# Optimization experiments

Measured on AMD Instinct MI355X. Metric: run time of the kernel, lower is better.

## Reference

```python
import jax, jax.numpy as jnp
import numpy as np

NEG_SLOPE = 0.2
N, E, R = 50000, 400000, 500
IN, HID, H, OUT = 128, 64, 4, 128


def _gatv2_layer(x, src, dst, e_emb, Wl, bl, Wr, br, att, bias, heads, ch, concat):
    """PyG GATv2Conv (eval mode, add_self_loops=True, fill_value=0.0)."""
    n = x.shape[0]
    xl = (x @ Wl + bl).reshape(n, heads, ch)   # source transform
    xr = (x @ Wr + br).reshape(n, heads, ch)   # destination transform
    loop = jnp.arange(n)
    src_f = jnp.concatenate([src, loop])       # self-loops appended
    dst_f = jnp.concatenate([dst, loop])
    # self-loop edge_attr is fill_value=0.0 -> lin_edge (no bias) gives 0 embedding
    e_f = jnp.concatenate([e_emb, jnp.zeros((n, heads, ch), x.dtype)], axis=0)
    m = jax.nn.leaky_relu(xl[src_f] + xr[dst_f] + e_f, NEG_SLOPE)  # [Ef,H,C]
    logits = jnp.einsum('ehc,hc->eh', m, att)
    # segment softmax over destination nodes (every node has a self loop)
    mx = jax.ops.segment_max(logits, dst_f, num_segments=n)
    a = jnp.exp(logits - mx[dst_f])
    denom = jax.ops.segment_sum(a, dst_f, num_segments=n)
    alpha = a / denom[dst_f]                                        # [Ef,H]
    out = jax.ops.segment_sum(alpha[..., None] * xl[src_f], dst_f, num_segments=n)
    if concat:
        out = out.reshape(n, heads * ch)
    else:
        out = out.mean(axis=1)
    return out + bias


def setup_inputs() -> dict:
    key = jax.random.key(0)
    ks = jax.random.split(key, 20)
    s = 0.05
    inp = {
        'x': jax.random.normal(ks[0], (N, IN), jnp.float32),
        'edge_index': jnp.stack([
            jax.random.randint(ks[1], (E,), 0, N),
            jax.random.randint(ks[2], (E,), 0, R),
            jax.random.randint(ks[3], (E,), 0, N),
        ]).astype(jnp.int64) if jax.config.jax_enable_x64 else jnp.stack([
            jax.random.randint(ks[1], (E,), 0, N),
            jax.random.randint(ks[2], (E,), 0, R),
            jax.random.randint(ks[3], (E,), 0, N),
        ]),
        'relations': jax.random.normal(ks[4], (R, IN), jnp.float32),
        # layer 1: IN -> H*HID, concat=True
        'Wl1': jax.random.normal(ks[5], (IN, H * HID), jnp.float32) * s,
        'bl1': jnp.zeros((H * HID,), jnp.float32),
        'Wr1': jax.random.normal(ks[6], (IN, H * HID), jnp.float32) * s,
        'br1': jnp.zeros((H * HID,), jnp.float32),
        'We1': jax.random.normal(ks[7], (IN, H * HID), jnp.float32) * s,
        'att1': jax.random.normal(ks[8], (H, HID), jnp.float32) * s,
        'bias1': jnp.zeros((H * HID,), jnp.float32),
        # layer 2: H*HID -> OUT, concat=False (mean over heads)
        'Wl2': jax.random.normal(ks[9], (H * HID, H * OUT), jnp.float32) * s,
        'bl2': jnp.zeros((H * OUT,), jnp.float32),
        'Wr2': jax.random.normal(ks[10], (H * HID, H * OUT), jnp.float32) * s,
        'br2': jnp.zeros((H * OUT,), jnp.float32),
        'We2': jax.random.normal(ks[11], (IN, H * OUT), jnp.float32) * s,
        'att2': jax.random.normal(ks[12], (H, OUT), jnp.float32) * s,
        'bias2': jnp.zeros((OUT,), jnp.float32),
    }
    return inp


def reference(x, edge_index, relations,
              Wl1, bl1, Wr1, br1, We1, att1, bias1,
              Wl2, bl2, Wr2, br2, We2, att2, bias2):
    src, rel, dst = edge_index[0], edge_index[1], edge_index[2]
    edge_attr = relations[rel]                                  # [E, IN]
    e1 = (edge_attr @ We1).reshape(-1, H, HID)
    h = _gatv2_layer(x, src, dst, e1, Wl1, bl1, Wr1, br1, att1, bias1, H, HID, True)
    e2 = (edge_attr @ We2).reshape(-1, H, OUT)
    out = _gatv2_layer(h, src, dst, e2, Wl2, bl2, Wr2, br2, att2, bias2, H, OUT, False)
    return out
```

## Files before the change

### kernel.cpp

```cpp
#include <hip/hip_runtime.h>
#include <math.h>

constexpr int NN   = 50000;
constexpr int NE   = 400000;
constexpr int NR   = 500;
constexpr int INF_ = 128;
constexpr int HIDC = 64;
constexpr int NH   = 4;
constexpr int OUTC = 128;
constexpr int MPAD = 50048;

typedef __attribute__((ext_vector_type(2))) _Float16 h2;
typedef __attribute__((ext_vector_type(4))) _Float16 h4;
typedef __attribute__((ext_vector_type(8))) _Float16 h8;
typedef __attribute__((ext_vector_type(4))) float f32x4;

__device__ __forceinline__ h2 b2(float f) {
    _Float16 h = (_Float16)f;
    return (h2){h, h};
}

__device__ __forceinline__ h2 lrelu2(h2 x) {
    h2 t = x * (h2){(_Float16)0.2f, (_Float16)0.2f};
#if __has_builtin(__builtin_elementwise_max)
    return __builtin_elementwise_max(x, t);
#else
    h2 r;
    r[0] = x[0] > t[0] ? x[0] : t[0];
    r[1] = x[1] > t[1] ? x[1] : t[1];
    return r;
#endif
}

__device__ __forceinline__ float fdot2a(h2 a, h2 b, float c) {
#if __has_builtin(__builtin_amdgcn_fdot2)
    return __builtin_amdgcn_fdot2(a, b, c, false);
#else
    return c + (float)a[0] * (float)b[0] + (float)a[1] * (float)b[1];
#endif
}

template <int NP>
__device__ __forceinline__ void load_h(const _Float16* p, h2* d) {
    if constexpr (NP == 2) {
        h4 t = *(const h4*)p;
        d[0] = (h2){t[0], t[1]}; d[1] = (h2){t[2], t[3]};
    } else {
        h8 t = *(const h8*)p;
        d[0] = (h2){t[0], t[1]}; d[1] = (h2){t[2], t[3]};
        d[2] = (h2){t[4], t[5]}; d[3] = (h2){t[6], t[7]};
    }
}

__device__ __forceinline__ void gl2lds16(const void* g, void* l) {
    __builtin_amdgcn_global_load_lds(
        (const __attribute__((address_space(1))) unsigned int*)g,
        (__attribute__((address_space(3))) unsigned int*)l, 16, 0, 0);
}

__global__ __launch_bounds__(256) void gemm_mfma(
    const _Float16* __restrict__ A,
    const _Float16* __restrict__ Bt,
    const float* __restrict__ bias,
    _Float16* __restrict__ C0, _Float16* __restrict__ C1,
    int M, int N, int K, int ntn)
{
    __shared__ __align__(16) char smem[128 * 144 * 2];
    _Float16* As = (_Float16*)smem;
    _Float16* Bs = (_Float16*)(smem + 16384);
    const int tid  = threadIdx.x;
    const int lane = tid & 63;
    const int wave = tid >> 6;

    const int nwg = gridDim.x;
    const int q = nwg >> 3, r = nwg & 7;
    const int xcd = blockIdx.x & 7, jj = blockIdx.x >> 3;
    const int swid = (xcd < r ? xcd * (q + 1) : r * (q + 1) + (xcd - r) * q) + jj;
    const int brow = (swid / ntn) * 128;
    const int bcol = (swid % ntn) * 128;

    f32x4 acc[4][4] = {};
    const int wr = (wave >> 1) * 64;
    const int wc = (wave & 1) * 64;
    const int swz = (lane >> 4) ^ ((lane >> 1) & 3);

    const int s0 = wave * 64 + lane;
    const int s1 = 256 + wave * 64 + lane;
    const int row0 = s0 >> 2, kc0 = (s0 & 3) ^ ((s0 >> 3) & 3);
    const int row1 = s1 >> 2, kc1 = (s1 & 3) ^ ((s1 >> 3) & 3);
    const _Float16* a0 = A + (size_t)(brow + row0) * K + kc0 * 8;
    const _Float16* a1 = A + (size_t)(brow + row1) * K + kc1 * 8;
    const _Float16* b0 = Bt + (size_t)(bcol + row0) * K + kc0 * 8;
    const _Float16* b1 = Bt + (size_t)(bcol + row1) * K + kc1 * 8;

#define STAGE(buf, k0) do {                                          \
        gl2lds16(a0 + (k0), &As[(buf) * 4096 + wave * 512]);         \
        gl2lds16(b0 + (k0), &Bs[(buf) * 4096 + wave * 512]);         \
        gl2lds16(a1 + (k0), &As[(buf) * 4096 + 2048 + wave * 512]);  \
        gl2lds16(b1 + (k0), &Bs[(buf) * 4096 + 2048 + wave * 512]);  \
    } while (0)

    STAGE(0, 0);
    const int nt = K >> 5;
    int cur = 0;
    for (int t = 0; t < nt; ++t) {
        if (t + 1 < nt) {
            STAGE(cur ^ 1, (t + 1) * 32);
            asm volatile("s_waitcnt vmcnt(4)" ::: "memory");
        } else {
            asm volatile("s_waitcnt vmcnt(0)" ::: "memory");
        }
        __builtin_amdgcn_s_barrier();
        __builtin_amdgcn_sched_barrier(0);
        h8 af[4], bfr[4];
        #pragma unroll
        for (int m = 0; m < 4; ++m)
            af[m] = *(const h8*)&As[cur * 4096 + (wr + m * 16 + (lane & 15)) * 32 + swz * 8];
        #pragma unroll
        for (int n = 0; n < 4; ++n)
            bfr[n] = *(const h8*)&Bs[cur * 4096 + (wc + n * 16 + (lane & 15)) * 32 + swz * 8];
        #pragma unroll
        for (int m = 0; m < 4; ++m)
            #pragma unroll
            for (int n = 0; n < 4; ++n)
                acc[m][n] = __builtin_amdgcn_mfma_f32_16x16x32_f16(
                    af[m], bfr[n], acc[m][n], 0, 0, 0);
        __builtin_amdgcn_s_barrier();
        cur ^= 1;
    }
#undef STAGE

    __syncthreads();
    _Float16* Cs = (_Float16*)smem;
    #pragma unroll
    for (int m = 0; m < 4; ++m) {
        int rl0 = wr + m * 16 + (lane >> 4) * 4;
        #pragma unroll
        for (int n = 0; n < 4; ++n) {
            int cl = wc + n * 16 + (lane & 15);
            float bv = bias ? bias[bcol + cl] : 0.f;
            #pragma unroll
            for (int j = 0; j < 4; ++j)
                Cs[(rl0 + j) * 144 + cl] = (_Float16)(acc[m][n][j] + bv);
        }
    }
    __syncthreads();

    const int half = N >> 1;
    const int c8 = (tid & 15) * 8;
    #pragma unroll
    for (int p = 0; p < 8; ++p) {
        int rl = p * 16 + (tid >> 4);
        int rr = brow + rl;
        if (rr >= M) continue;
        h8 vv = *(const h8*)&Cs[rl * 144 + c8];
        int c = bcol + c8;
        if (C1) {
            if (c < half) *(h8*)&C0[(size_t)rr * half + c] = vv;
            else          *(h8*)&C1[(size_t)rr * half + (c - half)] = vv;
        } else {
            *(h8*)&C0[(size_t)rr * N + c] = vv;
        }
    }
}

__global__ __launch_bounds__(256) void prep_all(
    const float* __restrict__ x,
    const float* __restrict__ Wl1, const float* __restrict__ Wr1,
    const float* __restrict__ Wl2, const float* __restrict__ Wr2,
    const float* __restrict__ We1, const float* __restrict__ We2,
    const float* __restrict__ relations,
    const float* __restrict__ bl1, const float* __restrict__ br1,
    const float* __restrict__ bl2, const float* __restrict__ br2,
    _Float16* __restrict__ xh, _Float16* __restrict__ hh,
    _Float16* __restrict__ Bt1, _Float16* __restrict__ Bt2,
    _Float16* __restrict__ BtE, _Float16* __restrict__ relh,
    float* __restrict__ pb1, float* __restrict__ pb2)
{
    constexpr long SXV   = (long)NN * INF_ / 4;
    constexpr long nXP   = (long)(MPAD - NN) * 128;
    constexpr long nHP   = (long)(MPAD - NN) * 256;
    constexpr long nW1   = 128 * 256;
    constexpr long nW2   = 256 * 512;
    constexpr long nWe1  = 128 * 256;
    constexpr long nWe2  = 128 * 512;
    constexpr long nRel  = (long)NR * 128;
    constexpr long nRelP = (512 - NR) * 128;
    constexpr long TOT = SXV + nXP + nHP + 2 * nW1 + 2 * nW2 + nWe1 + nWe2
                       + nRel + nRelP + 512 + 1024;

    for (long i = (long)blockIdx.x * 256 + threadIdx.x; i < TOT;
         i += (long)gridDim.x * 256) {
        long j = i;
        if (j < SXV) {
            float4 v = ((const float4*)x)[j];
            h4 o = {(_Float16)v.x, (_Float16)v.y, (_Float16)v.z, (_Float16)v.w};
            ((h4*)xh)[j] = o;
            continue;
        }
        j -= SXV;
        if (j < nXP) { xh[(long)NN * 128 + j] = (_Float16)0.f; continue; }
        j -= nXP;
        if (j < nHP) { hh[(long)NN * 256 + j] = (_Float16)0.f; continue; }
        j -= nHP;
        if (j < nW1) { long k = j >> 8, n = j & 255; Bt1[n * 128 + k] = (_Float16)Wl1[j]; continue; }
        j -= nW1;
        if (j < nW1) { long k = j >> 8, n = j & 255; Bt1[(256 + n) * 128 + k] = (_Float16)Wr1[j]; continue; }
        j -= nW1;
        if (j < nW2) { long k = j >> 9, n = j & 511; Bt2[n * 256 + k] = (_Float16)Wl2[j]; continue; }
        j -= nW2;
        if (j < nW2) { long k = j >> 9, n = j & 511; Bt2[(512 + n) * 256 + k] = (_Float16)Wr2[j]; continue; }
        j -= nW2;
        if (j < nWe1) { long k = j >> 8, n = j & 255; BtE[n * 128 + k] = (_Float16)We1[j]; continue; }
        j -= nWe1;
        if (j < nWe2) { long k = j >> 9, n = j & 511; BtE[(256 + n) * 128 + k] = (_Float16)We2[j]; continue; }
        j -= nWe2;
        if (j < nRel) { relh[j] = (_Float16)relations[j]; continue; }
        j -= nRel;
        if (j < nRelP) { relh[nRel + j] = (_Float16)0.f; continue; }
        j -= nRelP;
        if (j < 512) { pb1[j] = (j < 256) ? bl1[j] : br1[j - 256]; continue; }
        j -= 512;
        pb2[j] = (j < 512) ? bl2[j] : br2[j - 512];
    }
}

__global__ void count_deg(const int* __restrict__ dst, int* __restrict__ deg, int E)
{
    int i = blockIdx.x * blockDim.x + threadIdx.x;
    if (i < E) atomicAdd(&deg[dst[i]], 1);
}

__global__ __launch_bounds__(256) void scan_block_sums(
    const int* __restrict__ deg, int* __restrict__ bsum, int n)
{
    __shared__ int s[256];
    int i = blockIdx.x * 256 + threadIdx.x;
    s[threadIdx.x] = (i < n) ? deg[i] : 0;
    __syncthreads();
    for (int o = 128; o > 0; o >>= 1) {
        if (threadIdx.x < o) s[threadIdx.x] += s[threadIdx.x + o];
        __syncthreads();
    }
    if (threadIdx.x == 0) bsum[blockIdx.x] = s[0];
}

__global__ __launch_bounds__(256) void scan_bsums(
    const int* __restrict__ bsum, int* __restrict__ boff, int nb)
{
    __shared__ int s[256];
    int v = (threadIdx.x < nb) ? bsum[threadIdx.x] : 0;
    s[threadIdx.x] = v;
    __syncthreads();
    for (int o = 1; o < 256; o <<= 1) {
        int t = (threadIdx.x >= o) ? s[threadIdx.x - o] : 0;
        __syncthreads();
        s[threadIdx.x] += t;
        __syncthreads();
    }
    if (threadIdx.x < nb) boff[threadIdx.x] = s[threadIdx.x] - v;
}

__global__ __launch_bounds__(256) void scan_final(
    const int* __restrict__ deg, const int* __restrict__ boff,
    int* __restrict__ offsets, int n)
{
    __shared__ int s[256];
    int i = blockIdx.x * 256 + threadIdx.x;
    int v = (i < n) ? deg[i] : 0;
    s[threadIdx.x] = v;
    __syncthreads();
    for (int o = 1; o < 256; o <<= 1) {
        int t = (threadIdx.x >= o) ? s[threadIdx.x - o] : 0;
        __syncthreads();
        s[threadIdx.x] += t;
        __syncthreads();
    }
    int incl = s[threadIdx.x];
    int excl = incl - v;
    if (i < n) offsets[i] = boff[blockIdx.x] + excl;
    if (i == n - 1) offsets[n] = boff[blockIdx.x] + incl;
}

__global__ void fill_adj(const int* __restrict__ src, const int* __restrict__ rel,
                         const int* __restrict__ dst, const int* __restrict__ offsets,
                         int* __restrict__ cursor,
                         int2* __restrict__ adj, int E)
{
    int e = blockIdx.x * blockDim.x + threadIdx.x;
    if (e < E) {
        int d = dst[e];
        int p = atomicAdd(&cursor[d], 1);
        adj[offsets[d] + p] = make_int2(src[e], rel[e]);
    }
}

template <int CPH, bool CONCAT>
__global__ __launch_bounds__(64) void gat_node(
    const _Float16* __restrict__ xl,
    const _Float16* __restrict__ xr,
    const _Float16* __restrict__ erel,
    int ldE,
    const int2* __restrict__ adj,
    const int* __restrict__ offsets,
    const float* __restrict__ att,
    const float* __restrict__ bias,
    void* __restrict__ out, int n)
{
    constexpr int HC  = NH * CPH;
    constexpr int VPL = HC / 64;
    constexpr int NP  = VPL / 2;
    const int lane = threadIdx.x;
    const int v = blockIdx.x;
    if (v >= n) return;
    const int loff = lane * VPL;

    h2 xlv[NP], xrv[NP], attp[NP], acc[NP];
    load_h<NP>(xl + (size_t)v * HC + loff, xlv);
    load_h<NP>(xr + (size_t)v * HC + loff, xrv);
    #pragma unroll
    for (int p = 0; p < NP; ++p) {
        attp[p][0] = (_Float16)att[loff + 2 * p];
        attp[p][1] = (_Float16)att[loff + 2 * p + 1];
        acc[p] = xlv[p];
    }

    float pS = 0.f;
    #pragma unroll
    for (int p = 0; p < NP; ++p) pS = fdot2a(lrelu2(xlv[p] + xrv[p]), attp[p], pS);
    pS += __shfl_xor(pS, 1);
    pS += __shfl_xor(pS, 2);
    pS += __shfl_xor(pS, 4);
    pS += __shfl_xor(pS, 8);
    float m_run = pS, l_run = 1.f;

    const int beg = offsets[v], end = offsets[v + 1];
    int idx = beg;

    for (; idx + 8 <= end; idx += 8) {
        int2 ed[8];
        #pragma unroll
        for (int k = 0; k < 8; ++k) ed[k] = adj[idx + k];
        h2 xs[8][NP], ee[8][NP];
        #pragma unroll
        for (int k = 0; k < 8; ++k) {
            load_h<NP>(xl + (size_t)ed[k].x * HC + loff, xs[k]);
            load_h<NP>(erel + (size_t)ed[k].y * ldE + loff, ee[k]);
        }
        float pp[8] = {};
        #pragma unroll
        for (int p = 0; p < NP; ++p)
            #pragma unroll
            for (int k = 0; k < 8; ++k)
                pp[k] = fdot2a(lrelu2(xs[k][p] + xrv[p] + ee[k][p]), attp[p], pp[k]);
        #pragma unroll
        for (int msk = 1; msk <= 8; msk <<= 1)
            #pragma unroll
            for (int k = 0; k < 8; ++k) pp[k] += __shfl_xor(pp[k], msk);
        float mx = m_run;
        #pragma unroll
        for (int k = 0; k < 8; ++k) mx = fmaxf(mx, pp[k]);
        float sc = __expf(m_run - mx);
        float w[8], lsum = 0.f;
        #pragma unroll
        for (int k = 0; k < 8; ++k) { w[k] = __expf(pp[k] - mx); lsum += w[k]; }
        l_run = l_run * sc + lsum;
        h2 sc2 = b2(sc);
        #pragma unroll
        for (int p = 0; p < NP; ++p) {
            h2 a = acc[p] * sc2;
            #pragma unroll
            for (int k = 0; k < 8; ++k) a += xs[k][p] * b2(w[k]);
            acc[p] = a;
        }
        m_run = mx;
    }

    for (; idx + 4 <= end; idx += 4) {
        int2 ed[4];
        #pragma unroll
        for (int k = 0; k < 4; ++k) ed[k] = adj[idx + k];
        h2 xs[4][NP], ee[4][NP];
        #pragma unroll
        for (int k = 0; k < 4; ++k) {
            load_h<NP>(xl + (size_t)ed[k].x * HC + loff, xs[k]);
            load_h<NP>(erel + (size_t)ed[k].y * ldE + loff, ee[k]);
        }
        float pp[4] = {};
        #pragma unroll
        for (int p = 0; p < NP; ++p)
            #pragma unroll
            for (int k = 0; k < 4; ++k)
                pp[k] = fdot2a(lrelu2(xs[k][p] + xrv[p] + ee[k][p]), attp[p], pp[k]);
        #pragma unroll
        for (int msk = 1; msk <= 8; msk <<= 1)
            #pragma unroll
            for (int k = 0; k < 4; ++k) pp[k] += __shfl_xor(pp[k], msk);
        float mx = m_run;
        #pragma unroll
        for (int k = 0; k < 4; ++k) mx = fmaxf(mx, pp[k]);
        float sc = __expf(m_run - mx);
        float w[4], lsum = 0.f;
        #pragma unroll
        for (int k = 0; k < 4; ++k) { w[k] = __expf(pp[k] - mx); lsum += w[k]; }
        l_run = l_run * sc + lsum;
        h2 sc2 = b2(sc);
        #pragma unroll
        for (int p = 0; p < NP; ++p) {
            h2 a = acc[p] * sc2;
            #pragma unroll
            for (int k = 0; k < 4; ++k) a += xs[k][p] * b2(w[k]);
            acc[p] = a;
        }
        m_run = mx;
    }

    for (; idx < end; ++idx) {
        int2 ed = adj[idx];
        h2 xs0[NP], e0[NP];
        load_h<NP>(xl + (size_t)ed.x * HC + loff, xs0);
        load_h<NP>(erel + (size_t)ed.y * ldE + loff, e0);
        float p0 = 0.f;
        #pragma unroll
        for (int p = 0; p < NP; ++p)
            p0 = fdot2a(lrelu2(xs0[p] + xrv[p] + e0[p]), attp[p], p0);
        p0 += __shfl_xor(p0, 1);
        p0 += __shfl_xor(p0, 2);
        p0 += __shfl_xor(p0, 4);
        p0 += __shfl_xor(p0, 8);
        float mx = fmaxf(m_run, p0);
        float sc = __expf(m_run - mx);
        float w0 = __expf(p0 - mx);
        l_run = l_run * sc + w0;
        h2 sc2 = b2(sc), w02 = b2(w0);
        #pragma unroll
        for (int p = 0; p < NP; ++p) acc[p] = acc[p] * sc2 + xs0[p] * w02;
        m_run = mx;
    }

    float inv = 1.f / l_run;
    if constexpr (CONCAT) {
        _Float16* ob = (_Float16*)out + (size_t)v * HC + loff;
        if constexpr (NP == 2) {
            h4 o;
            #pragma unroll
            for (int p = 0; p < NP; ++p) {
                o[2 * p]     = (_Float16)((float)acc[p][0] * inv + bias[loff + 2 * p]);
                o[2 * p + 1] = (_Float16)((float)acc[p][1] * inv + bias[loff + 2 * p + 1]);
            }
            *(h4*)ob = o;
        } else {
            h8 o;
            #pragma unroll
            for (int p = 0; p < NP; ++p) {
                o[2 * p]     = (_Float16)((float)acc[p][0] * inv + bias[loff + 2 * p]);
                o[2 * p + 1] = (_Float16)((float)acc[p][1] * inv + bias[loff + 2 * p + 1]);
            }
            *(h8*)ob = o;
        }
    } else {
        float* of = (float*)out;
        float t[VPL];
        #pragma unroll
        for (int j = 0; j < VPL; ++j) {
            t[j] = (float)acc[j / 2][j & 1] * inv;
            t[j] += __shfl_xor(t[j], 16);
            t[j] += __shfl_xor(t[j], 32);
        }
        if (lane < 16) {
            #pragma unroll
            for (int j = 0; j < VPL; ++j)
                of[(size_t)v * CPH + lane * VPL + j] = 0.25f * t[j] + bias[lane * VPL + j];
        }
    }
}

extern "C" void kernel_launch(void* const* d_in, const int* in_sizes, int n_in,
                              void* d_out, int out_size, void* d_ws, size_t ws_size,
                              hipStream_t stream)
{
    const float* x         = (const float*)d_in[0];
    const int*   ei        = (const int*)d_in[1];
    const float* relations = (const float*)d_in[2];
    const float* Wl1  = (const float*)d_in[3];
    const float* bl1  = (const float*)d_in[4];
    const float* Wr1  = (const float*)d_in[5];
    const float* br1  = (const float*)d_in[6];
    const float* We1  = (const float*)d_in[7];
    const float* att1 = (const float*)d_in[8];
    const float* bias1= (const float*)d_in[9];
    const float* Wl2  = (const float*)d_in[10];
    const float* bl2  = (const float*)d_in[11];
    const float* Wr2  = (const float*)d_in[12];
    const float* br2  = (const float*)d_in[13];
    const float* We2  = (const float*)d_in[14];
    const float* att2 = (const float*)d_in[15];
    const float* bias2= (const float*)d_in[16];
    float* out = (float*)d_out;

    const int* src = ei;
    const int* rel = ei + NE;
    const int* dst = ei + 2 * NE;

    _Float16* xh   = (_Float16*)d_ws;
    _Float16* hh   = xh + (size_t)MPAD * 128;
    _Float16* xl1  = hh + (size_t)MPAD * 256;
    _Float16* xr1  = xl1 + (size_t)NN * 256;
    _Float16* xl2  = xr1 + (size_t)NN * 256;
    _Float16* xr2  = xl2 + (size_t)NN * 512;
    _Float16* Bt1  = xr2 + (size_t)NN * 512;
    _Float16* Bt2  = Bt1 + 512 * 128;
    _Float16* BtE  = Bt2 + 1024 * 256;
    _Float16* relh = BtE + 768 * 128;
    _Float16* erelC= relh + 512 * 128;
    float* pb1     = (float*)(erelC + 512 * 768);
    float* pb2     = pb1 + 512;
    int* deg     = (int*)(pb2 + 1024);
    int* cursor  = deg + NN;
    int* offsets = cursor + NN;
    int* bsum    = offsets + NN + 1;
    int* boff    = bsum + 256;
    int2* adj    = (int2*)(boff + 256);

    const int NB = (NN + 255) / 256;
    const int EB = (NE + 255) / 256;

    hipMemsetAsync(deg, 0, (size_t)2 * NN * sizeof(int), stream);

    prep_all<<<2048, 256, 0, stream>>>(x, Wl1, Wr1, Wl2, Wr2, We1, We2, relations,
                                       bl1, br1, bl2, br2,
                                       xh, hh, Bt1, Bt2, BtE, relh, pb1, pb2);

    count_deg<<<EB, 256, 0, stream>>>(dst, deg, NE);
    scan_block_sums<<<NB, 256, 0, stream>>>(deg, bsum, NN);
    scan_bsums<<<1, 256, 0, stream>>>(bsum, boff, NB);
    scan_final<<<NB, 256, 0, stream>>>(deg, boff, offsets, NN);
    fill_adj<<<EB, 256, 0, stream>>>(src, rel, dst, offsets, cursor, adj, NE);

    gemm_mfma<<<4 * 6, 256, 0, stream>>>(relh, BtE, nullptr, erelC, nullptr,
                                         NR, 768, 128, 6);

    gemm_mfma<<<(MPAD / 128) * 4, 256, 0, stream>>>(xh, Bt1, pb1, xl1, xr1,
                                                    NN, 512, 128, 4);

    gat_node<HIDC, true><<<NN, 64, 0, stream>>>(
        xl1, xr1, erelC, 768, adj, offsets, att1, bias1, hh, NN);

    gemm_mfma<<<(MPAD / 128) * 8, 256, 0, stream>>>(hh, Bt2, pb2, xl2, xr2,
                                                    NN, 1024, 256, 8);

    gat_node<OUTC, false><<<NN, 64, 0, stream>>>(
        xl2, xr2, erelC + 256, 768, adj, offsets, att2, bias2, out, NN);
}
```

Before: 257.0 us.

## Fuse degree counting into prep kernel, drop pad zeroing and 8-edge unroll

The degree-count atomics move into the grid-stride prep_all kernel, removing one kernel launch. The zero-fill of GEMM padding rows (xh, hh, relh) is dropped, on the assumption that padded rows only produce outputs that are never read. The 8-edge unrolled loop in the GAT node kernel is removed, so edges are handled in batches of 4 plus a remainder. This should cut register pressure, but it exposes fewer gathers in flight per iteration, and leaving padding uninitialised relies on those rows never reaching valid results.

Result: faster. 248.3 us (-3.4%).

```diff
diff --git a/kernel.cpp b/kernel.cpp
--- a/kernel.cpp
+++ b/kernel.cpp
@@ -172,22 +172,20 @@
     const float* __restrict__ relations,
     const float* __restrict__ bl1, const float* __restrict__ br1,
     const float* __restrict__ bl2, const float* __restrict__ br2,
-    _Float16* __restrict__ xh, _Float16* __restrict__ hh,
+    const int* __restrict__ dst, int* __restrict__ deg,
+    _Float16* __restrict__ xh,
     _Float16* __restrict__ Bt1, _Float16* __restrict__ Bt2,
     _Float16* __restrict__ BtE, _Float16* __restrict__ relh,
     float* __restrict__ pb1, float* __restrict__ pb2)
 {
     constexpr long SXV   = (long)NN * INF_ / 4;
-    constexpr long nXP   = (long)(MPAD - NN) * 128;
-    constexpr long nHP   = (long)(MPAD - NN) * 256;
     constexpr long nW1   = 128 * 256;
     constexpr long nW2   = 256 * 512;
     constexpr long nWe1  = 128 * 256;
     constexpr long nWe2  = 128 * 512;
     constexpr long nRel  = (long)NR * 128;
-    constexpr long nRelP = (512 - NR) * 128;
-    constexpr long TOT = SXV + nXP + nHP + 2 * nW1 + 2 * nW2 + nWe1 + nWe2
-                       + nRel + nRelP + 512 + 1024;
+    constexpr long TOT = SXV + 2 * nW1 + 2 * nW2 + nWe1 + nWe2
+                       + nRel + 512 + 1024 + NE;
 
     for (long i = (long)blockIdx.x * 256 + threadIdx.x; i < TOT;
          i += (long)gridDim.x * 256) {
@@ -199,10 +197,6 @@
             continue;
         }
         j -= SXV;
-        if (j < nXP) { xh[(long)NN * 128 + j] = (_Float16)0.f; continue; }
-        j -= nXP;
-        if (j < nHP) { hh[(long)NN * 256 + j] = (_Float16)0.f; continue; }
-        j -= nHP;
         if (j < nW1) { long k = j >> 8, n = j & 255; Bt1[n * 128 + k] = (_Float16)Wl1[j]; continue; }
         j -= nW1;
         if (j < nW1) { long k = j >> 8, n = j & 255; Bt1[(256 + n) * 128 + k] = (_Float16)Wr1[j]; continue; }
@@ -217,18 +211,12 @@
         j -= nWe2;
         if (j < nRel) { relh[j] = (_Float16)relations[j]; continue; }
         j -= nRel;
-        if (j < nRelP) { relh[nRel + j] = (_Float16)0.f; continue; }
-        j -= nRelP;
         if (j < 512) { pb1[j] = (j < 256) ? bl1[j] : br1[j - 256]; continue; }
         j -= 512;
-        pb2[j] = (j < 512) ? bl2[j] : br2[j - 512];
-    }
-}
-
-__global__ void count_deg(const int* __restrict__ dst, int* __restrict__ deg, int E)
-{
-    int i = blockIdx.x * blockDim.x + threadIdx.x;
-    if (i < E) atomicAdd(&deg[dst[i]], 1);
+        if (j < 1024) { pb2[j] = (j < 512) ? bl2[j] : br2[j - 512]; continue; }
+        j -= 1024;
+        atomicAdd(&deg[dst[j]], 1);
+    }
 }
 
 __global__ __launch_bounds__(256) void scan_block_sums(
@@ -336,46 +324,6 @@
 
     const int beg = offsets[v], end = offsets[v + 1];
     int idx = beg;
-
-    for (; idx + 8 <= end; idx += 8) {
-        int2 ed[8];
-        #pragma unroll
-        for (int k = 0; k < 8; ++k) ed[k] = adj[idx + k];
-        h2 xs[8][NP], ee[8][NP];
-        #pragma unroll
-        for (int k = 0; k < 8; ++k) {
-            load_h<NP>(xl + (size_t)ed[k].x * HC + loff, xs[k]);
-            load_h<NP>(erel + (size_t)ed[k].y * ldE + loff, ee[k]);
-        }
-        float pp[8] = {};
-        #pragma unroll
-        for (int p = 0; p < NP; ++p)
-            #pragma unroll
-            for (int k = 0; k < 8; ++k)
-                pp[k] = fdot2a(lrelu2(xs[k][p] + xrv[p] + ee[k][p]), attp[p], pp[k]);
-        #pragma unroll
-        for (int msk = 1; msk <= 8; msk <<= 1)
-            #pragma unroll
-            for (int k = 0; k < 8; ++k) pp[k] += __shfl_xor(pp[k], msk);
-        float mx = m_run;
-        #pragma unroll
-        for (int k = 0; k < 8; ++k) mx = fmaxf(mx, pp[k]);
-        float sc = __expf(m_run - mx);
-        float w[8], lsum = 0.f;
-        #pragma unroll
-        for (int k = 0; k < 8; ++k) { w[k] = __expf(pp[k] - mx); lsum += w[k]; }
-        l_run = l_run * sc + lsum;
-        h2 sc2 = b2(sc);
-        #pragma unroll
-        for (int p = 0; p < NP; ++p) {
-            h2 a = acc[p] * sc2;
-            #pragma unroll
-            for (int k = 0; k < 8; ++k) a += xs[k][p] * b2(w[k]);
-            acc[p] = a;
-        }
-        m_run = mx;
-    }
-
     for (; idx + 4 <= end; idx += 4) {
         int2 ed[4];
         #pragma unroll
@@ -414,7 +362,6 @@
         }
         m_run = mx;
     }
-
     for (; idx < end; ++idx) {
         int2 ed = adj[idx];
         h2 xs0[NP], e0[NP];
@@ -528,10 +475,9 @@
     hipMemsetAsync(deg, 0, (size_t)2 * NN * sizeof(int), stream);
 
     prep_all<<<2048, 256, 0, stream>>>(x, Wl1, Wr1, Wl2, Wr2, We1, We2, relations,
-                                       bl1, br1, bl2, br2,
-                                       xh, hh, Bt1, Bt2, BtE, relh, pb1, pb2);
-
-    count_deg<<<EB, 256, 0, stream>>>(dst, deg, NE);
+                                       bl1, br1, bl2, br2, dst, deg,
+                                       xh, Bt1, Bt2, BtE, relh, pb1, pb2);
+
     scan_block_sums<<<NB, 256, 0, stream>>>(deg, bsum, NN);
     scan_bsums<<<1, 256, 0, stream>>>(bsum, boff, NB);
     scan_final<<<NB, 256, 0, stream>>>(deg, boff, offsets, NN);
```
